# Optimization experiments

Measured on AMD Instinct MI355X. Metric: run time of the kernel, lower is better.

The kernel has to match this reference:

```python
import jax, jax.numpy as jnp
import numpy as np
import math

H = 16
D_MODEL = 1024
LEN_Q = 2048
LEN_K = 2048
D_K = 64
D_V = 64
B = 4
NEG = -1000000000.0


def setup_inputs() -> dict:
    key = jax.random.key(0)
    ks = jax.random.split(key, 9)
    Q = jax.random.normal(ks[0], (B, LEN_Q, D_MODEL), dtype=jnp.float32)
    K = jax.random.normal(ks[1], (B, LEN_K, D_MODEL), dtype=jnp.float32)
    V = jax.random.normal(ks[2], (B, LEN_K, D_MODEL), dtype=jnp.float32)
    mask = jax.random.randint(ks[3], (B, LEN_K), 0, 2, dtype=jnp.int32)
    s = 1.0 / math.sqrt(D_MODEL)
    Wq = jax.random.normal(ks[4], (H * D_K, D_MODEL), dtype=jnp.float32) * s
    bq = jnp.zeros((H * D_K,), dtype=jnp.float32)
    Wk = jax.random.normal(ks[5], (H * D_K, D_MODEL), dtype=jnp.float32) * s
    Wv = jax.random.normal(ks[6], (H * D_V, D_MODEL), dtype=jnp.float32) * s
    bv = jnp.zeros((H * D_V,), dtype=jnp.float32)
    return {"Q": Q, "K": K, "V": V, "mask": mask,
            "Wq": Wq, "bq": bq, "Wk": Wk, "Wv": Wv, "bv": bv}


def reference(Q, K, V, mask, Wq, bq, Wk, Wv, bv):
    scale = math.sqrt(float(D_K))
    # projections (W_Q, W_V have bias; W_K does not)
    q = (jnp.einsum('bsd,od->bso', Q, Wq) + bq).reshape(B, LEN_Q, H, D_K)
    k = jnp.einsum('bsd,od->bso', K, Wk).reshape(B, LEN_K, H, D_K)
    v = (jnp.einsum('bsd,od->bso', V, Wv) + bv).reshape(B, LEN_K, H, D_V)
    # scores [B, H, len_q, len_k]
    A = jnp.einsum('bqhd,bkhd->bhqk', q, k) / scale
    m = (mask != 0)[:, None, None, :]  # [B,1,1,len_k]
    A = jnp.where(m, A, A + 0.0)
    A = jnp.where(m, A, NEG)
    alpha = jax.nn.softmax(A, axis=-1)
    out = jnp.einsum('bhqk,bkhd->bqhd', alpha, v)  # [B, len_q, H, d_v]
    return out.reshape(B, LEN_Q, H * D_V)
```

## Files before the change

### kernel.cpp

```cpp
#include <hip/hip_runtime.h>
#include <stdint.h>
#include <math.h>

#define NH 16
#define DM 1024
#define SEQ 2048
#define DH 64
#define NB 4
#define NEG2 (-1.4426950408889634e9f)
#define SCL2 (0.18033688011112042f)

typedef __attribute__((ext_vector_type(8))) short bf16x8;
typedef __attribute__((ext_vector_type(4))) short bf16x4;
typedef __attribute__((ext_vector_type(4))) float f32x4;
typedef unsigned short u16;
typedef uint32_t u32;

__device__ __forceinline__ u16 f2bf(float f) {
    union { float f; u32 i; } c; c.f = f;
    u32 r = c.i + 0x7fffu + ((c.i >> 16) & 1u);
    return (u16)(r >> 16);
}
__device__ __forceinline__ u32 packbf(float lo, float hi) {
    union { float f; u32 i; } a, b; a.f = lo; b.f = hi;
    return ((a.i + 0x8000u) >> 16) | ((b.i + 0x8000u) & 0xFFFF0000u);
}

__device__ __forceinline__ float fexp2(float x) {
#if __has_builtin(__builtin_amdgcn_exp2f)
    return __builtin_amdgcn_exp2f(x);
#else
    return exp2f(x);
#endif
}

__device__ __forceinline__ f32x4 pv_mfma(bf16x4 a, bf16x4 b, f32x4 c) {
#if __has_builtin(__builtin_amdgcn_mfma_f32_16x16x16bf16_1k)
    return __builtin_amdgcn_mfma_f32_16x16x16bf16_1k(a, b, c, 0, 0, 0);
#else
    f32x4 d;
    asm volatile("s_nop 1\n\t"
                 "v_mfma_f32_16x16x16_bf16 %0, %1, %2, %3\n\t"
                 "s_nop 7\n\t"
                 "s_nop 7"
                 : "=v"(d) : "v"(a), "v"(b), "v"(c));
    return d;
#endif
}

__device__ __forceinline__ void gl_lds16(const u16* g, u16* l) {
#if __has_builtin(__builtin_amdgcn_global_load_lds)
    __builtin_amdgcn_global_load_lds(
        (const __attribute__((address_space(1))) void*)g,
        (__attribute__((address_space(3))) void*)l, 16, 0, 0);
#else
    *(uint4*)(l + (threadIdx.x & 63) * 8) = *(const uint4*)(g);
#endif
}

__global__ __launch_bounds__(256) void cvt_kernel(const float* __restrict__ src,
                                                  u16* __restrict__ dst, int n4) {
    int i = blockIdx.x * 256 + threadIdx.x;
    if (i >= n4) return;
    float4 v = ((const float4*)src)[i];
    ushort4 o = { f2bf(v.x), f2bf(v.y), f2bf(v.z), f2bf(v.w) };
    ((ushort4*)dst)[i] = o;
}

__global__ __launch_bounds__(256) void prep_kernel(
    const float* __restrict__ Wq, const float* __restrict__ Wk,
    const float* __restrict__ Wv, const int* __restrict__ mask,
    u16* __restrict__ wqb, u16* __restrict__ wkb, u16* __restrict__ wvb,
    float* __restrict__ mf) {
    const int bid = blockIdx.x;
    if (bid < 3072) {
        const float* src = (bid < 1024) ? Wq : (bid < 2048) ? Wk : Wv;
        u16* dst = (bid < 1024) ? wqb : (bid < 2048) ? wkb : wvb;
        int i = (bid & 1023) * 256 + threadIdx.x;
        float4 v = ((const float4*)src)[i];
        ushort4 o = { f2bf(v.x), f2bf(v.y), f2bf(v.z), f2bf(v.w) };
        ((ushort4*)dst)[i] = o;
    } else {
        int i = (bid - 3072) * 256 + threadIdx.x;
        mf[i] = mask[i] ? 0.0f : NEG2;
    }
}

__global__ __launch_bounds__(256, 2) void proj_kernel(
    const u16* __restrict__ X, const u16* __restrict__ W,
    const float* __restrict__ bias, u16* __restrict__ out, int vt)
{
    __shared__ __align__(16) u16 sbuf[2][16384];
    const int p   = blockIdx.y * 8 + blockIdx.x;
    const int xcd = p & 7;
    const int i8  = p >> 3;
    const int ly  = xcd * 8 + (i8 >> 3);
    const int lx  = i8 & 7;

    const int tid  = threadIdx.x;
    const int lane = tid & 63;
    const int wave = tid >> 6;
    const int row  = lane & 15;
    const int quad = lane >> 4;
    const int n0 = lx * 128;
    const int m0 = ly * 128;
    const int wm = (wave & 1) * 64;
    const int wn = (wave >> 1) * 64;

    const int r0 = wave * 16 + (lane >> 2);
    const int c0 = (lane & 3) ^ ((r0 >> 1) & 3);
    const u16* xg0 = X + (size_t)(m0 + r0) * DM + c0 * 8;
    const u16* xg1 = xg0 + (size_t)64 * DM;
    const u16* wg0 = W + (size_t)(n0 + r0) * DM + c0 * 8;
    const u16* wg1 = wg0 + (size_t)64 * DM;
    const int la0 = wave * 512;

    const int rsw = (quad ^ ((row >> 1) & 3)) * 8;

#define STAGE(bsel, kt) do {                                 \
        u16* ab = &sbuf[bsel][la0];                          \
        gl_lds16(xg0 + (kt),        ab);                     \
        gl_lds16(xg1 + (kt),        ab + 2048);              \
        gl_lds16(xg0 + (kt) + 32,   ab + 4096);              \
        gl_lds16(xg1 + (kt) + 32,   ab + 6144);              \
        gl_lds16(wg0 + (kt),        ab + 8192);              \
        gl_lds16(wg1 + (kt),        ab + 10240);             \
        gl_lds16(wg0 + (kt) + 32,   ab + 12288);             \
        gl_lds16(wg1 + (kt) + 32,   ab + 14336);             \
    } while (0)

    f32x4 acc[4][4] = {};
    STAGE(0, 0);
    for (int ki = 0; ki < 16; ++ki) {
        __syncthreads();
        if (ki < 15) STAGE((ki + 1) & 1, (ki + 1) * 64);

        const u16* buf = sbuf[ki & 1];
#pragma unroll
        for (int ks = 0; ks < 2; ++ks) {
            const u16* Ab = buf + ks * 4096;
            const u16* Bb = buf + 8192 + ks * 4096;
            bf16x8 af[4], bfr[4];
#pragma unroll
            for (int i = 0; i < 4; i++)
                af[i] = *(const bf16x8*)(Ab + (wm + i * 16 + row) * 32 + rsw);
#pragma unroll
            for (int j = 0; j < 4; j++)
                bfr[j] = *(const bf16x8*)(Bb + (wn + j * 16 + row) * 32 + rsw);
#pragma unroll
            for (int i = 0; i < 4; i++)
#pragma unroll
                for (int j = 0; j < 4; j++)
                    acc[i][j] = __builtin_amdgcn_mfma_f32_16x16x32_bf16(af[i], bfr[j], acc[i][j], 0, 0, 0);
        }
    }
#undef STAGE

    const int bidx = m0 >> 11;
#pragma unroll
    for (int j = 0; j < 4; j++) {
        const int n = n0 + wn + j * 16 + row;
        const int h = n >> 6;
        const int c = n & (DH - 1);
        const float bvv = bias ? bias[n] : 0.0f;
#pragma unroll
        for (int i = 0; i < 4; i++) {
            const int mbase = m0 + wm + i * 16 + quad * 4;
            const int s = mbase & (SEQ - 1);
            if (vt) {
                ushort4 o = { f2bf(acc[i][j][0] + bvv), f2bf(acc[i][j][1] + bvv),
                              f2bf(acc[i][j][2] + bvv), f2bf(acc[i][j][3] + bvv) };
                size_t idx = (((size_t)(bidx * NH + h) * 32 + (s >> 6)) * DH + c) * 64 + (s & 63);
                *(ushort4*)(out + idx) = o;
            } else {
#pragma unroll
                for (int r = 0; r < 4; r++)
                    out[(size_t)((bidx * NH + h) * SEQ + s + r) * DH + c] = f2bf(acc[i][j][r] + bvv);
            }
        }
    }
}

__global__ __launch_bounds__(256, 3) void attn_kernel(
    const u16* __restrict__ qws, const u16* __restrict__ kws,
    const u16* __restrict__ vws, const float* __restrict__ maskf,
    float* __restrict__ out)
{
    __shared__ __align__(16) u16 kbuf[2][64 * 72];
    __shared__ __align__(16) u16 vbuf[2][64 * 72];
    const int tid  = threadIdx.x;
    const int lane = tid & 63;
    const int wave = tid >> 6;
    const int row  = lane & 15;
    const int quad = lane >> 4;
    const int bid = blockIdx.x;
    const int qb = bid & 15;
    const int h  = (bid >> 4) & (NH - 1);
    const int b  = bid >> 8;
    const int q0 = qb * 128 + wave * 32;

    const u16* qbase = qws + (size_t)(b * NH + h) * SEQ * DH;
    const u16* kbase = kws + (size_t)(b * NH + h) * SEQ * DH;
    const u16* vtb   = vws + (size_t)(b * NH + h) * 32 * (DH * 64);
    const float* mrow = maskf + b * SEQ;

    const int srow = tid >> 3;
    const int scol = (tid & 7) * 8;
    const u16* kgp = kbase + (size_t)srow * DH + scol;
    const int ldso = srow * 72 + scol;
    const int vldso = ldso;

    bf16x8 qf[2][2];
#pragma unroll
    for (int gi = 0; gi < 2; gi++) {
        qf[gi][0] = *(const bf16x8*)(qbase + (size_t)(q0 + gi * 16 + row) * DH + quad * 8);
        qf[gi][1] = *(const bf16x8*)(qbase + (size_t)(q0 + gi * 16 + row) * DH + 32 + quad * 8);
    }

    f32x4 O[2][4] = {};
    float lrun[2] = {0.0f, 0.0f};

    {
        uint4 k0 = *(const uint4*)(kgp);
        uint4 k1 = *(const uint4*)(kgp + (size_t)32 * DH);
        uint4 v0 = *(const uint4*)(vtb + tid * 8);
        uint4 v1 = *(const uint4*)(vtb + (tid + 256) * 8);
        *(uint4*)(&kbuf[0][ldso])            = k0;
        *(uint4*)(&kbuf[0][32 * 72 + ldso])  = k1;
        *(uint4*)(&vbuf[0][vldso])           = v0;
        *(uint4*)(&vbuf[0][32 * 72 + vldso]) = v1;
    }

    for (int it = 0; it < 32; ++it) {
        const int kt = it * 64;
        __syncthreads();
        float4 mk[4];
#pragma unroll
        for (int g = 0; g < 4; g++)
            mk[g] = *(const float4*)(mrow + kt + g * 16 + quad * 4);
        const int itn = (it == 31) ? 0 : it + 1;
        uint4 kr0 = *(const uint4*)(kgp + (size_t)itn * 64 * DH);
        uint4 kr1 = *(const uint4*)(kgp + (size_t)(itn * 64 + 32) * DH);
        uint4 vr0 = *(const uint4*)(vtb + (size_t)itn * 4096 + tid * 8);
        uint4 vr1 = *(const uint4*)(vtb + (size_t)itn * 4096 + (tid + 256) * 8);

        const u16* kb = kbuf[it & 1];
        f32x4 st[2][4] = {};
#pragma unroll
        for (int g = 0; g < 4; g++) {
#pragma unroll
            for (int ks = 0; ks < 2; ks++) {
                bf16x8 kf = *(const bf16x8*)(kb + (g * 16 + row) * 72 + ks * 32 + quad * 8);
                st[0][g] = __builtin_amdgcn_mfma_f32_16x16x32_bf16(kf, qf[0][ks], st[0][g], 0, 0, 0);
                st[1][g] = __builtin_amdgcn_mfma_f32_16x16x32_bf16(kf, qf[1][ks], st[1][g], 0, 0, 0);
            }
        }

        union { u32 u[2]; bf16x4 v; } pw[2][4];
#pragma unroll
        for (int gi = 0; gi < 2; gi++) {
            float lsum = 0.0f;
#pragma unroll
            for (int g = 0; g < 4; g++) {
                float p0 = fexp2(fmaf(st[gi][g][0], SCL2, mk[g].x));
                float p1 = fexp2(fmaf(st[gi][g][1], SCL2, mk[g].y));
                float p2 = fexp2(fmaf(st[gi][g][2], SCL2, mk[g].z));
                float p3 = fexp2(fmaf(st[gi][g][3], SCL2, mk[g].w));
                lsum += (p0 + p1) + (p2 + p3);
                pw[gi][g].u[0] = packbf(p0, p1);
                pw[gi][g].u[1] = packbf(p2, p3);
            }
            lsum += __shfl_xor(lsum, 16, 64);
            lsum += __shfl_xor(lsum, 32, 64);
            lrun[gi] += lsum;
        }

        const u16* vb = vbuf[it & 1];
#pragma unroll
        for (int dg = 0; dg < 4; dg++) {
#pragma unroll
            for (int g = 0; g < 4; g++) {
                bf16x4 vfrag = *(const bf16x4*)(vb + (dg * 16 + row) * 72 + g * 16 + quad * 4);
                O[0][dg] = pv_mfma(vfrag, pw[0][g].v, O[0][dg]);
                O[1][dg] = pv_mfma(vfrag, pw[1][g].v, O[1][dg]);
            }
        }

        u16* nkb = kbuf[(it + 1) & 1];
        u16* nvb = vbuf[(it + 1) & 1];
        *(uint4*)(nkb + ldso)             = kr0;
        *(uint4*)(nkb + 32 * 72 + ldso)   = kr1;
        *(uint4*)(nvb + vldso)            = vr0;
        *(uint4*)(nvb + 32 * 72 + vldso)  = vr1;
    }

#pragma unroll
    for (int gi = 0; gi < 2; gi++) {
        const float rl = 1.0f / lrun[gi];
        const int q = q0 + gi * 16 + row;
#pragma unroll
        for (int dg = 0; dg < 4; dg++) {
            float4 o4 = { O[gi][dg][0] * rl, O[gi][dg][1] * rl,
                          O[gi][dg][2] * rl, O[gi][dg][3] * rl };
            *(float4*)(out + (size_t)(b * SEQ + q) * (NH * DH) + h * DH + dg * 16 + quad * 4) = o4;
        }
    }
}

extern "C" void kernel_launch(void* const* d_in, const int* in_sizes, int n_in,
                              void* d_out, int out_size, void* d_ws, size_t ws_size,
                              hipStream_t stream) {
    const float* Q    = (const float*)d_in[0];
    const float* K    = (const float*)d_in[1];
    const float* V    = (const float*)d_in[2];
    const int*   mask = (const int*)d_in[3];
    const float* Wq   = (const float*)d_in[4];
    const float* bq   = (const float*)d_in[5];
    const float* Wk   = (const float*)d_in[6];
    const float* Wv   = (const float*)d_in[7];
    const float* bv   = (const float*)d_in[8];
    float* out = (float*)d_out;

    const size_t XN = (size_t)NB * SEQ * DM;
    const size_t WN = (size_t)DM * DM;
    u16* ws = (u16*)d_ws;
    u16* xbuf = ws;
    u16* wqb  = ws + XN;
    u16* wkb  = wqb + WN;
    u16* wvb  = wkb + WN;
    u16* qws  = wvb + WN;
    u16* kws  = qws + XN;
    u16* vws  = kws + XN;
    float* maskf = (float*)(vws + XN);

    dim3 blk(256);
    const int gX = (int)(XN / 4 / 256);
    dim3 pgrid(DM / 128, NB * SEQ / 128);

    prep_kernel<<<3072 + 32, blk, 0, stream>>>(Wq, Wk, Wv, mask, wqb, wkb, wvb, maskf);

    cvt_kernel<<<gX, blk, 0, stream>>>(K, xbuf, (int)(XN / 4));
    proj_kernel<<<pgrid, blk, 0, stream>>>(xbuf, wkb, nullptr, kws, 0);
    cvt_kernel<<<gX, blk, 0, stream>>>(V, xbuf, (int)(XN / 4));
    proj_kernel<<<pgrid, blk, 0, stream>>>(xbuf, wvb, bv, vws, 1);
    cvt_kernel<<<gX, blk, 0, stream>>>(Q, xbuf, (int)(XN / 4));
    proj_kernel<<<pgrid, blk, 0, stream>>>(xbuf, wqb, bq, qws, 0);

    attn_kernel<<<dim3(NB * NH * (SEQ / 128)), blk, 0, stream>>>(qws, kws, vws, maskf, out);
}
```

Baseline: 336.4 us.

## Batch all input conversions and Q/K/V projections into single merged launches

```diff
diff --git a/kernel.cpp b/kernel.cpp
--- a/kernel.cpp
+++ b/kernel.cpp
@@ -70,8 +70,11 @@
 __global__ __launch_bounds__(256) void prep_kernel(
     const float* __restrict__ Wq, const float* __restrict__ Wk,
     const float* __restrict__ Wv, const int* __restrict__ mask,
+    const float* __restrict__ Q, const float* __restrict__ K,
+    const float* __restrict__ V,
     u16* __restrict__ wqb, u16* __restrict__ wkb, u16* __restrict__ wvb,
-    float* __restrict__ mf) {
+    float* __restrict__ mf,
+    u16* __restrict__ qxb, u16* __restrict__ kxb, u16* __restrict__ vxb) {
     const int bid = blockIdx.x;
     if (bid < 3072) {
         const float* src = (bid < 1024) ? Wq : (bid < 2048) ? Wk : Wv;
@@ -80,9 +83,115 @@
         float4 v = ((const float4*)src)[i];
         ushort4 o = { f2bf(v.x), f2bf(v.y), f2bf(v.z), f2bf(v.w) };
         ((ushort4*)dst)[i] = o;
-    } else {
+    } else if (bid < 3104) {
         int i = (bid - 3072) * 256 + threadIdx.x;
         mf[i] = mask[i] ? 0.0f : NEG2;
+    } else {
+        const int r = bid - 3104;
+        const float* src = (r < 8192) ? Q : (r < 16384) ? K : V;
+        u16* dst = (r < 8192) ? qxb : (r < 16384) ? kxb : vxb;
+        int i = (r & 8191) * 256 + threadIdx.x;
+        float4 v = ((const float4*)src)[i];
+        ushort4 o = { f2bf(v.x), f2bf(v.y), f2bf(v.z), f2bf(v.w) };
+        ((ushort4*)dst)[i] = o;
+    }
+}
+
+__global__ __launch_bounds__(256, 4) void projm_kernel(
+    const u16* __restrict__ qxb, const u16* __restrict__ kxb,
+    const u16* __restrict__ vxb,
+    const u16* __restrict__ wqb, const u16* __restrict__ wkb,
+    const u16* __restrict__ wvb,
+    const float* __restrict__ bq, const float* __restrict__ bv,
+    u16* __restrict__ qo, u16* __restrict__ ko, u16* __restrict__ vo)
+{
+    __shared__ __align__(16) u16 sbuf[2][8192];
+    const int p   = blockIdx.y * 8 + blockIdx.x;
+    const int xcd = p & 7;
+    const int i8  = p >> 3;
+    const int ly  = xcd * 24 + (i8 >> 3);
+    const int lx  = i8 & 7;
+
+    const int which = ly >> 6;
+    const u16* X  = (which == 0) ? qxb : (which == 1) ? kxb : vxb;
+    const u16* W  = (which == 0) ? wqb : (which == 1) ? wkb : wvb;
+    const float* bias = (which == 0) ? bq : (which == 2) ? bv : nullptr;
+    u16* out = (which == 0) ? qo : (which == 1) ? ko : vo;
+    const int vt = (which == 2);
+
+    const int tid  = threadIdx.x;
+    const int lane = tid & 63;
+    const int wave = tid >> 6;
+    const int row  = lane & 15;
+    const int quad = lane >> 4;
+    const int n0 = lx * 128;
+    const int m0 = (ly & 63) * 128;
+    const int wm = (wave & 1) * 64;
+    const int wn = (wave >> 1) * 64;
+
+    const int r0 = wave * 16 + (lane >> 2);
+    const int c0 = (lane & 3) ^ ((r0 >> 1) & 3);
+    const u16* xg0 = X + (size_t)(m0 + r0) * DM + c0 * 8;
+    const u16* xg1 = xg0 + (size_t)64 * DM;
+    const u16* wg0 = W + (size_t)(n0 + r0) * DM + c0 * 8;
+    const u16* wg1 = wg0 + (size_t)64 * DM;
+    const int la0 = wave * 512;
+
+    const int rsw = (quad ^ ((row >> 1) & 3)) * 8;
+
+#define STAGE(bsel, kt) do {                         \
+        u16* ab = &sbuf[bsel][la0];                  \
+        gl_lds16(xg0 + (kt), ab);                    \
+        gl_lds16(xg1 + (kt), ab + 2048);             \
+        gl_lds16(wg0 + (kt), ab + 4096);             \
+        gl_lds16(wg1 + (kt), ab + 6144);             \
+    } while (0)
+
+    f32x4 acc[4][4] = {};
+    STAGE(0, 0);
+    for (int ki = 0; ki < 32; ++ki) {
+        __syncthreads();
+        if (ki < 31) STAGE((ki + 1) & 1, (ki + 1) * 32);
+
+        const u16* Ab = sbuf[ki & 1];
+        const u16* Bb = Ab + 4096;
+        bf16x8 af[4], bfr[4];
+#pragma unroll
+        for (int i = 0; i < 4; i++)
+            af[i] = *(const bf16x8*)(Ab + (wm + i * 16 + row) * 32 + rsw);
+#pragma unroll
+        for (int j = 0; j < 4; j++)
+            bfr[j] = *(const bf16x8*)(Bb + (wn + j * 16 + row) * 32 + rsw);
+#pragma unroll
+        for (int i = 0; i < 4; i++)
+#pragma unroll
+            for (int j = 0; j < 4; j++)
+                acc[i][j] = __builtin_amdgcn_mfma_f32_16x16x32_bf16(af[i], bfr[j], acc[i][j], 0, 0, 0);
+    }
+#undef STAGE
+
+    const int bidx = m0 >> 11;
+#pragma unroll
+    for (int j = 0; j < 4; j++) {
+        const int n = n0 + wn + j * 16 + row;
+        const int h = n >> 6;
+        const int c = n & (DH - 1);
+        const float bvv = bias ? bias[n] : 0.0f;
+#pragma unroll
+        for (int i = 0; i < 4; i++) {
+            const int mbase = m0 + wm + i * 16 + quad * 4;
+            const int s = mbase & (SEQ - 1);
+            if (vt) {
+                ushort4 o = { f2bf(acc[i][j][0] + bvv), f2bf(acc[i][j][1] + bvv),
+                              f2bf(acc[i][j][2] + bvv), f2bf(acc[i][j][3] + bvv) };
+                size_t idx = (((size_t)(bidx * NH + h) * 32 + (s >> 6)) * DH + c) * 64 + (s & 63);
+                *(ushort4*)(out + idx) = o;
+            } else {
+#pragma unroll
+                for (int r = 0; r < 4; r++)
+                    out[(size_t)((bidx * NH + h) * SEQ + s + r) * DH + c] = f2bf(acc[i][j][r] + bvv);
+            }
+        }
     }
 }
 
@@ -193,7 +302,8 @@
     const int wave = tid >> 6;
     const int row  = lane & 15;
     const int quad = lane >> 4;
-    const int bid = blockIdx.x;
+    const int bid0 = blockIdx.x;
+    const int bid  = ((bid0 & 7) << 7) | (bid0 >> 3);
     const int qb = bid & 15;
     const int h  = (bid >> 4) & (NH - 1);
     const int b  = bid >> 8;
@@ -323,28 +433,57 @@
 
     const size_t XN = (size_t)NB * SEQ * DM;
     const size_t WN = (size_t)DM * DM;
-    u16* ws = (u16*)d_ws;
-    u16* xbuf = ws;
-    u16* wqb  = ws + XN;
-    u16* wkb  = wqb + WN;
-    u16* wvb  = wkb + WN;
-    u16* qws  = wvb + WN;
-    u16* kws  = qws + XN;
-    u16* vws  = kws + XN;
-    float* maskf = (float*)(vws + XN);
-
     dim3 blk(256);
-    const int gX = (int)(XN / 4 / 256);
-    dim3 pgrid(DM / 128, NB * SEQ / 128);
-
-    prep_kernel<<<3072 + 32, blk, 0, stream>>>(Wq, Wk, Wv, mask, wqb, wkb, wvb, maskf);
-
-    cvt_kernel<<<gX, blk, 0, stream>>>(K, xbuf, (int)(XN / 4));
-    proj_kernel<<<pgrid, blk, 0, stream>>>(xbuf, wkb, nullptr, kws, 0);
-    cvt_kernel<<<gX, blk, 0, stream>>>(V, xbuf, (int)(XN / 4));
-    proj_kernel<<<pgrid, blk, 0, stream>>>(xbuf, wvb, bv, vws, 1);
-    cvt_kernel<<<gX, blk, 0, stream>>>(Q, xbuf, (int)(XN / 4));
-    proj_kernel<<<pgrid, blk, 0, stream>>>(xbuf, wqb, bq, qws, 0);
-
-    attn_kernel<<<dim3(NB * NH * (SEQ / 128)), blk, 0, stream>>>(qws, kws, vws, maskf, out);
-}
+
+    const size_t need_full = (6 * XN + 3 * WN) * 2 + 32768;
+
+    if (ws_size >= need_full) {
+        u16* ws   = (u16*)d_ws;
+        u16* qxb  = ws;
+        u16* kxb  = qxb + XN;
+        u16* vxb  = kxb + XN;
+        u16* wqb  = vxb + XN;
+        u16* wkb  = wqb + WN;
+        u16* wvb  = wkb + WN;
+        u16* qws  = wvb + WN;
+        u16* kws  = qws + XN;
+        u16* vws  = kws + XN;
+        float* maskf = (float*)(vws + XN);
+
+        prep_kernel<<<3104 + 3 * 8192, blk, 0, stream>>>(
+            Wq, Wk, Wv, mask, Q, K, V, wqb, wkb, wvb, maskf, qxb, kxb, vxb);
+
+        projm_kernel<<<dim3(8, 192), blk, 0, stream>>>(
+            qxb, kxb, vxb, wqb, wkb, wvb, bq, bv, qws, kws, vws);
+
+        attn_kernel<<<dim3(NB * NH * (SEQ / 128)), blk, 0, stream>>>(
+            qws, kws, vws, maskf, out);
+    } else {
+        u16* ws   = (u16*)d_ws;
+        u16* xbuf = ws;
+        u16* wqb  = ws + XN;
+        u16* wkb  = wqb + WN;
+        u16* wvb  = wkb + WN;
+        u16* qws  = wvb + WN;
+        u16* kws  = qws + XN;
+        u16* vws  = kws + XN;
+        float* maskf = (float*)(vws + XN);
+
+        const int gX = (int)(XN / 4 / 256);
+        dim3 pgrid(DM / 128, NB * SEQ / 128);
+
+        prep_kernel<<<3104, blk, 0, stream>>>(
+            Wq, Wk, Wv, mask, Q, K, V, wqb, wkb, wvb, maskf,
+            nullptr, nullptr, nullptr);
+
+        cvt_kernel<<<gX, blk, 0, stream>>>(K, xbuf, (int)(XN / 4));
+        proj_kernel<<<pgrid, blk, 0, stream>>>(xbuf, wkb, nullptr, kws, 0);
+        cvt_kernel<<<gX, blk, 0, stream>>>(V, xbuf, (int)(XN / 4));
+        proj_kernel<<<pgrid, blk, 0, stream>>>(xbuf, wvb, bv, vws, 1);
+        cvt_kernel<<<gX, blk, 0, stream>>>(Q, xbuf, (int)(XN / 4));
+        proj_kernel<<<pgrid, blk, 0, stream>>>(xbuf, wqb, bq, qws, 0);
+
+        attn_kernel<<<dim3(NB * NH * (SEQ / 128)), blk, 0, stream>>>(
+            qws, kws, vws, maskf, out);
+    }
+}
```

New measurement: 327.4 us (median of 2 runs). 1.03x faster.
